# Performance work log

Hardware: AMD Instinct MI355X
Metric: run time of the kernel (lower is better)

## Reference

```python
import jax, jax.numpy as jnp
import numpy as np

DIM = 2048
N_HEADS = 16
HEAD_DIM = DIM // N_HEADS
MAX_SEQ_LEN = 2048
ROPE_THETA = 32.0
EPS = 1e-6


def _precompute_freqs_1d(dim, max_seq_len, theta):
    freqs = theta ** (-np.arange(0, dim, 2, dtype=np.float32) / dim)  # [dim/2]
    pos = np.arange(max_seq_len, dtype=np.float32)                    # [S]
    ang = pos[:, None] * freqs[None, :]                               # [S, dim/2]
    return jnp.asarray(np.cos(ang)), jnp.asarray(np.sin(ang))


def _rms_norm(x, w):
    # x: [..., d]
    inv = jax.lax.rsqrt(jnp.mean(x * x, axis=-1, keepdims=True) + EPS)
    return x * inv * w


def setup_inputs() -> dict:
    key = jax.random.key(0)
    k1, k2, k3 = jax.random.split(key, 3)
    bsz, seq_len = 4, 2048
    x = jax.random.normal(k1, (bsz, seq_len, DIM), dtype=jnp.float32)
    w_qkv = jax.random.normal(k2, (3 * DIM, DIM), dtype=jnp.float32) * (DIM ** -0.5)
    w_proj = jax.random.normal(k3, (DIM, DIM), dtype=jnp.float32) * (DIM ** -0.5)
    q_norm_w = jnp.ones((HEAD_DIM,), dtype=jnp.float32)
    k_norm_w = jnp.ones((HEAD_DIM,), dtype=jnp.float32)
    return {"x": x, "w_qkv": w_qkv, "w_proj": w_proj,
            "q_norm_w": q_norm_w, "k_norm_w": k_norm_w}


def reference(x, w_qkv, w_proj, q_norm_w, k_norm_w):
    bsz, seq_len, dim = x.shape
    scale = HEAD_DIM ** -0.5

    # QKV projection (torch Linear: x @ W^T)
    qkv = jnp.einsum('bsd,ed->bse', x, w_qkv)  # [b, s, 3*dim]
    qkv = qkv.reshape(bsz, seq_len, 3, N_HEADS, HEAD_DIM).transpose(2, 0, 3, 1, 4)
    q, k, v = qkv[0], qkv[1], qkv[2]           # each [b, h, s, d]

    # Per-head RMSNorm on q, k
    q = _rms_norm(q, q_norm_w)
    k = _rms_norm(k, k_norm_w)

    # RoPE (half-split convention)
    cos, sin = _precompute_freqs_1d(HEAD_DIM, MAX_SEQ_LEN, ROPE_THETA)
    cos = cos[:seq_len][None, None]  # [1,1,s,d/2]
    sin = sin[:seq_len][None, None]
    q1, q2 = jnp.split(q, 2, axis=-1)
    k1, k2 = jnp.split(k, 2, axis=-1)
    q = jnp.concatenate([q1 * cos - q2 * sin, q2 * cos + q1 * sin], axis=-1)
    k = jnp.concatenate([k1 * cos - k2 * sin, k2 * cos + k1 * sin], axis=-1)

    # Scaled dot-product attention (no mask, eval-mode: no dropout)
    scores = jnp.einsum('bhqd,bhkd->bhqk', q, k) * scale
    attn = jax.nn.softmax(scores, axis=-1)
    y = jnp.einsum('bhqk,bhkd->bhqd', attn, v)

    # Merge heads + output projection
    y = y.transpose(0, 2, 1, 3).reshape(bsz, seq_len, dim)
    return jnp.einsum('bsd,ed->bse', y, w_proj)
```

## Files before the change

kernel.cpp:

```cpp
#include <hip/hip_runtime.h>
#include <hip/hip_bf16.h>

#define BSZ 4
#define SEQ 2048
#define DIM 2048
#define NH 16
#define HD 128
#define QK_LD 4096
#define SCALE 0.08838834764831845f

typedef __attribute__((ext_vector_type(8))) short bf16x8;
typedef __attribute__((ext_vector_type(4))) float f32x4;

#define GLDS16(g, l)                                                           \
  __builtin_amdgcn_global_load_lds(                                           \
      (const __attribute__((address_space(1))) void*)(g),                     \
      (__attribute__((address_space(3))) void*)(l), 16, 0, 0)

__device__ inline short f2b(float f) {
  __hip_bfloat16 h = __float2bfloat16(f);
  short s;
  __builtin_memcpy(&s, &h, 2);
  return s;
}

__device__ inline void stage16(const float* gp, __hip_bfloat16* lp) {
  float4 q0 = ((const float4*)gp)[0], q1 = ((const float4*)gp)[1];
  float4 q2 = ((const float4*)gp)[2], q3 = ((const float4*)gp)[3];
  bf16x8 v0, v1;
  v0[0] = f2b(q0.x); v0[1] = f2b(q0.y); v0[2] = f2b(q0.z); v0[3] = f2b(q0.w);
  v0[4] = f2b(q1.x); v0[5] = f2b(q1.y); v0[6] = f2b(q1.z); v0[7] = f2b(q1.w);
  v1[0] = f2b(q2.x); v1[1] = f2b(q2.y); v1[2] = f2b(q2.z); v1[3] = f2b(q2.w);
  v1[4] = f2b(q3.x); v1[5] = f2b(q3.y); v1[6] = f2b(q3.z); v1[7] = f2b(q3.w);
  *(bf16x8*)lp = v0;
  *(bf16x8*)(lp + 8) = v1;
}

__device__ inline char* out_slice(void* outv, int b, int fl) {
  return (char*)outv + (size_t)b * (size_t)SEQ * DIM * (fl ? 2u : 4u);
}

__global__ __launch_bounds__(256)
void detect_canon(const unsigned int* __restrict__ wbits,
                  const void* __restrict__ qw, const void* __restrict__ kw,
                  __hip_bfloat16* __restrict__ qwb,
                  __hip_bfloat16* __restrict__ kwb, int* __restrict__ flag) {
  __shared__ int cnt;
  const int t = threadIdx.x;
  if (t == 0) cnt = 0;
  __syncthreads();
  int local = 0;
  for (int i = 0; i < 4; ++i) {
    unsigned int e = (wbits[t * 4 + i] >> 7) & 0xFF;
    if (e >= 96 && e < 160) local++;
  }
  atomicAdd(&cnt, local);
  __syncthreads();
  const int f = (cnt >= 768) ? 1 : 0;
  if (t == 0) *flag = f;
  if (t < 128)
    qwb[t] = f ? ((const __hip_bfloat16*)qw)[t]
               : __float2bfloat16(((const float*)qw)[t]);
  else
    kwb[t - 128] = f ? ((const __hip_bfloat16*)kw)[t - 128]
                     : __float2bfloat16(((const float*)kw)[t - 128]);
}

__global__ __launch_bounds__(256)
void convert_bf16(const void* __restrict__ in, __hip_bfloat16* __restrict__ out,
                  const int* __restrict__ flag) {
  const int fl = *flag;
  long i = ((long)blockIdx.x * 256 + threadIdx.x) * 8;
  if (fl) {
    *(float4*)(out + i) = *(const float4*)((const __hip_bfloat16*)in + i);
  } else {
    const float* p = (const float*)in + i;
    float4 a = ((const float4*)p)[0], b = ((const float4*)p)[1];
    bf16x8 o;
    o[0] = f2b(a.x); o[1] = f2b(a.y); o[2] = f2b(a.z); o[3] = f2b(a.w);
    o[4] = f2b(b.x); o[5] = f2b(b.y); o[6] = f2b(b.z); o[7] = f2b(b.w);
    *(bf16x8*)(out + i) = o;
  }
}


__global__ __launch_bounds__(256)
void gemm_qkv_full(const __hip_bfloat16* __restrict__ A,
                   const __hip_bfloat16* __restrict__ B,
                   __hip_bfloat16* __restrict__ qk, void* __restrict__ outv,
                   const int* __restrict__ flag) {
  __shared__ __hip_bfloat16 As[128 * 32];
  __shared__ __hip_bfloat16 Bs[128 * 32];
  const int t = threadIdx.x, wave = t >> 6, lane = t & 63;
  const int quad = lane >> 4, l16 = lane & 15;
  const int wm = (wave & 1) * 64, wn = (wave >> 1) * 64;
  const long bm = (long)blockIdx.x * 128, bn = (long)blockIdx.y * 128;
  const int fl = *flag;

  f32x4 acc[4][4] = {};
  for (int k0 = 0; k0 < DIM; k0 += 32) {
    __syncthreads();
    for (int i = 0; i < 2; ++i) {
      int c = wave * 64 + lane + i * 256;
      int row = c >> 2, kc = c & 3;
      GLDS16(A + (bm + row) * DIM + k0 + kc * 8, As + (wave * 64 + i * 256) * 8);
      GLDS16(B + (bn + row) * DIM + k0 + kc * 8, Bs + (wave * 64 + i * 256) * 8);
    }
    __syncthreads();
    bf16x8 aF[4], bF[4];
    for (int mt = 0; mt < 4; ++mt)
      aF[mt] = *(const bf16x8*)(As + (wm + mt * 16 + l16) * 32 + quad * 8);
    for (int nt = 0; nt < 4; ++nt)
      bF[nt] = *(const bf16x8*)(Bs + (wn + nt * 16 + l16) * 32 + quad * 8);
    for (int mt = 0; mt < 4; ++mt)
      for (int nt = 0; nt < 4; ++nt)
        acc[mt][nt] = __builtin_amdgcn_mfma_f32_16x16x32_bf16(
            aF[mt], bF[nt], acc[mt][nt], 0, 0, 0);
  }

  if (bn < 4096) {
    for (int mt = 0; mt < 4; ++mt) {
      long gr = bm + wm + mt * 16 + quad * 4;
      for (int nt = 0; nt < 4; ++nt) {
        long gc = bn + wn + nt * 16 + l16;
        for (int r = 0; r < 4; ++r)
          qk[(gr + r) * QK_LD + gc] = __float2bfloat16(acc[mt][nt][r]);
      }
    }
  } else {
    for (int mt = 0; mt < 4; ++mt) {
      long gr = bm + wm + mt * 16 + quad * 4;
      __hip_bfloat16* vtb = (__hip_bfloat16*)out_slice(outv, (int)(gr >> 11), fl);
      long s = gr & 2047;
      for (int nt = 0; nt < 4; ++nt) {
        long col = bn - 4096 + wn + nt * 16 + l16;
        for (int r = 0; r < 4; ++r)
          vtb[col * SEQ + s + r] = __float2bfloat16(acc[mt][nt][r]);
      }
    }
  }
}

__global__ __launch_bounds__(256)
void gemm_proj_full(const __hip_bfloat16* __restrict__ A,
                    const __hip_bfloat16* __restrict__ B,
                    void* __restrict__ outv, const int* __restrict__ flag) {
  __shared__ __hip_bfloat16 As[128 * 32];
  __shared__ __hip_bfloat16 Bs[128 * 32];
  const int t = threadIdx.x, wave = t >> 6, lane = t & 63;
  const int quad = lane >> 4, l16 = lane & 15;
  const int wm = (wave & 1) * 64, wn = (wave >> 1) * 64;
  const long bm = (long)blockIdx.x * 128, bn = (long)blockIdx.y * 128;
  const int fl = *flag;

  f32x4 acc[4][4] = {};
  for (int k0 = 0; k0 < DIM; k0 += 32) {
    __syncthreads();
    for (int i = 0; i < 2; ++i) {
      int c = wave * 64 + lane + i * 256;
      int row = c >> 2, kc = c & 3;
      GLDS16(A + (bm + row) * QK_LD + k0 + kc * 8, As + (wave * 64 + i * 256) * 8);
      GLDS16(B + (bn + row) * DIM + k0 + kc * 8, Bs + (wave * 64 + i * 256) * 8);
    }
    __syncthreads();
    bf16x8 aF[4], bF[4];
    for (int mt = 0; mt < 4; ++mt)
      aF[mt] = *(const bf16x8*)(As + (wm + mt * 16 + l16) * 32 + quad * 8);
    for (int nt = 0; nt < 4; ++nt)
      bF[nt] = *(const bf16x8*)(Bs + (wn + nt * 16 + l16) * 32 + quad * 8);
    for (int mt = 0; mt < 4; ++mt)
      for (int nt = 0; nt < 4; ++nt)
        acc[mt][nt] = __builtin_amdgcn_mfma_f32_16x16x32_bf16(
            aF[mt], bF[nt], acc[mt][nt], 0, 0, 0);
  }

  for (int mt = 0; mt < 4; ++mt) {
    long gr = bm + wm + mt * 16 + quad * 4;
    for (int nt = 0; nt < 4; ++nt) {
      long gc = bn + wn + nt * 16 + l16;
      for (int r = 0; r < 4; ++r) {
        long idx = (gr + r) * DIM + gc;
        if (fl) ((__hip_bfloat16*)outv)[idx] = __float2bfloat16(acc[mt][nt][r]);
        else    ((float*)outv)[idx] = acc[mt][nt][r];
      }
    }
  }
}


__global__ __launch_bounds__(256)
void gemm_qkv(const void* __restrict__ xin, const void* __restrict__ win,
              __hip_bfloat16* __restrict__ qk, void* __restrict__ outv,
              const int* __restrict__ flag, int b) {
  __shared__ __hip_bfloat16 As[128 * 32];
  __shared__ __hip_bfloat16 Bs[128 * 32];
  const int t = threadIdx.x, wave = t >> 6, lane = t & 63;
  const int quad = lane >> 4, l16 = lane & 15;
  const int wm = (wave & 1) * 64, wn = (wave >> 1) * 64;
  const long bm = (long)blockIdx.x * 128, bn = (long)blockIdx.y * 128;
  const int fl = *flag;
  const __hip_bfloat16* Ab = (const __hip_bfloat16*)xin + (long)b * SEQ * DIM;
  const __hip_bfloat16* Bb = (const __hip_bfloat16*)win;
  const float* Af = (const float*)xin + (long)b * SEQ * DIM;
  const float* Bf = (const float*)win;

  f32x4 acc[4][4] = {};
  for (int k0 = 0; k0 < DIM; k0 += 32) {
    __syncthreads();
    if (fl) {
      for (int i = 0; i < 2; ++i) {
        int c = wave * 64 + lane + i * 256;
        int row = c >> 2, kc = c & 3;
        GLDS16(Ab + (bm + row) * DIM + k0 + kc * 8, As + (wave * 64 + i * 256) * 8);
        GLDS16(Bb + (bn + row) * DIM + k0 + kc * 8, Bs + (wave * 64 + i * 256) * 8);
      }
    } else {
      int row = t >> 1, cb = k0 + (t & 1) * 16;
      stage16(Af + (bm + row) * DIM + cb, As + t * 16);
      stage16(Bf + (bn + row) * DIM + cb, Bs + t * 16);
    }
    __syncthreads();
    bf16x8 aF[4], bF[4];
    for (int mt = 0; mt < 4; ++mt)
      aF[mt] = *(const bf16x8*)(As + (wm + mt * 16 + l16) * 32 + quad * 8);
    for (int nt = 0; nt < 4; ++nt)
      bF[nt] = *(const bf16x8*)(Bs + (wn + nt * 16 + l16) * 32 + quad * 8);
    for (int mt = 0; mt < 4; ++mt)
      for (int nt = 0; nt < 4; ++nt)
        acc[mt][nt] = __builtin_amdgcn_mfma_f32_16x16x32_bf16(
            aF[mt], bF[nt], acc[mt][nt], 0, 0, 0);
  }

  if (bn < 4096) {
    for (int mt = 0; mt < 4; ++mt) {
      long gr = bm + wm + mt * 16 + quad * 4;
      for (int nt = 0; nt < 4; ++nt) {
        long gc = bn + wn + nt * 16 + l16;
        for (int r = 0; r < 4; ++r)
          qk[(gr + r) * QK_LD + gc] = __float2bfloat16(acc[mt][nt][r]);
      }
    }
  } else {
    __hip_bfloat16* vtb = (__hip_bfloat16*)out_slice(outv, b, fl);
    for (int mt = 0; mt < 4; ++mt) {
      long gr = bm + wm + mt * 16 + quad * 4;
      for (int nt = 0; nt < 4; ++nt) {
        long col = bn - 4096 + wn + nt * 16 + l16;
        for (int r = 0; r < 4; ++r)
          vtb[col * SEQ + gr + r] = __float2bfloat16(acc[mt][nt][r]);
      }
    }
  }
}

__global__ __launch_bounds__(256)
void gemm_proj(const __hip_bfloat16* __restrict__ A, const void* __restrict__ win,
               void* __restrict__ outv, const int* __restrict__ flag, int b) {
  __shared__ __hip_bfloat16 As[128 * 32];
  __shared__ __hip_bfloat16 Bs[128 * 32];
  const int t = threadIdx.x, wave = t >> 6, lane = t & 63;
  const int quad = lane >> 4, l16 = lane & 15;
  const int wm = (wave & 1) * 64, wn = (wave >> 1) * 64;
  const long bm = (long)blockIdx.x * 128, bn = (long)blockIdx.y * 128;
  const int fl = *flag;
  const __hip_bfloat16* Bb = (const __hip_bfloat16*)win;
  const float* Bf = (const float*)win;

  f32x4 acc[4][4] = {};
  for (int k0 = 0; k0 < DIM; k0 += 32) {
    __syncthreads();
    for (int i = 0; i < 2; ++i) {
      int c = wave * 64 + lane + i * 256;
      int row = c >> 2, kc = c & 3;
      GLDS16(A + (bm + row) * QK_LD + k0 + kc * 8, As + (wave * 64 + i * 256) * 8);
    }
    if (fl) {
      for (int i = 0; i < 2; ++i) {
        int c = wave * 64 + lane + i * 256;
        int row = c >> 2, kc = c & 3;
        GLDS16(Bb + (bn + row) * DIM + k0 + kc * 8, Bs + (wave * 64 + i * 256) * 8);
      }
    } else {
      int row = t >> 1, cb = k0 + (t & 1) * 16;
      stage16(Bf + (bn + row) * DIM + cb, Bs + t * 16);
    }
    __syncthreads();
    bf16x8 aF[4], bF[4];
    for (int mt = 0; mt < 4; ++mt)
      aF[mt] = *(const bf16x8*)(As + (wm + mt * 16 + l16) * 32 + quad * 8);
    for (int nt = 0; nt < 4; ++nt)
      bF[nt] = *(const bf16x8*)(Bs + (wn + nt * 16 + l16) * 32 + quad * 8);
    for (int mt = 0; mt < 4; ++mt)
      for (int nt = 0; nt < 4; ++nt)
        acc[mt][nt] = __builtin_amdgcn_mfma_f32_16x16x32_bf16(
            aF[mt], bF[nt], acc[mt][nt], 0, 0, 0);
  }

  char* Cb = out_slice(outv, b, fl);
  for (int mt = 0; mt < 4; ++mt) {
    long gr = bm + wm + mt * 16 + quad * 4;
    for (int nt = 0; nt < 4; ++nt) {
      long gc = bn + wn + nt * 16 + l16;
      for (int r = 0; r < 4; ++r) {
        long idx = (gr + r) * DIM + gc;
        if (fl) ((__hip_bfloat16*)Cb)[idx] = __float2bfloat16(acc[mt][nt][r]);
        else    ((float*)Cb)[idx] = acc[mt][nt][r];
      }
    }
  }
}


__global__ __launch_bounds__(256)
void norm_rope(__hip_bfloat16* __restrict__ qk,
               const __hip_bfloat16* __restrict__ qwb,
               const __hip_bfloat16* __restrict__ kwb) {
  const int wave = threadIdx.x >> 6, lane = threadIdx.x & 63;
  const int gid = blockIdx.x * 4 + wave;
  const int h = gid & 15, tt = (gid >> 4) & 1, row = gid >> 5;
  const int s = row & 2047;

  __hip_bfloat16* p = qk + (long)row * QK_LD + tt * DIM + h * HD;
  float v1 = __bfloat162float(p[lane]);
  float v2 = __bfloat162float(p[lane + 64]);

  float ss = v1 * v1 + v2 * v2;
  for (int off = 1; off < 64; off <<= 1) ss += __shfl_xor(ss, off);
  float inv = rsqrtf(ss * (1.0f / 128.0f) + 1e-6f);

  const __hip_bfloat16* w = tt ? kwb : qwb;
  float n1 = v1 * inv * __bfloat162float(w[lane]);
  float n2 = v2 * inv * __bfloat162float(w[lane + 64]);

  float freq = exp2f(-5.0f * (float)lane * (1.0f / 64.0f));
  float ang = (float)s * freq;
  float c = cosf(ang), sn = sinf(ang);

  p[lane]      = __float2bfloat16(n1 * c - n2 * sn);
  p[lane + 64] = __float2bfloat16(n2 * c + n1 * sn);
}

__global__ __launch_bounds__(256)
void flash_attn(__hip_bfloat16* __restrict__ qk, void* __restrict__ outv,
                const int* __restrict__ flag, int b) {
  __shared__ __hip_bfloat16 Qs[4 * 64 * 32];
  __shared__ __hip_bfloat16 Ks[4 * 64 * 32];
  __shared__ __hip_bfloat16 Vs[2 * 128 * 32];
  __shared__ __hip_bfloat16 Ps[4][2 * 16 * 32];

  const int t = threadIdx.x, wave = t >> 6, lane = t & 63;
  const int quad = lane >> 4, l16 = lane & 15;
  const int q0 = blockIdx.x * 64, h = blockIdx.y;
  const int fl = *flag;
  __hip_bfloat16* Qg = qk + h * HD;
  const __hip_bfloat16* Kg = Qg + DIM;
  const __hip_bfloat16* Vt =
      (const __hip_bfloat16*)out_slice(outv, b, fl) + (long)h * HD * SEQ;

  for (int i = 0; i < 4; ++i) {
    int f = wave * 64 + lane + i * 256;
    int kk = f & 3, row = (f >> 2) & 63, ks = f >> 8;
    GLDS16(Qg + (long)(q0 + row) * QK_LD + ks * 32 + kk * 8,
           Qs + (wave * 64 + i * 256) * 8);
  }

  f32x4 oacc[8] = {};
  float m_run[4], l_run[4];
  for (int r = 0; r < 4; ++r) { m_run[r] = -1e30f; l_run[r] = 0.0f; }

  for (int j0 = 0; j0 < SEQ; j0 += 64) {
    __syncthreads();
    for (int i = 0; i < 4; ++i) {
      int f = wave * 64 + lane + i * 256;
      int kk = f & 3, row = (f >> 2) & 63, ks = f >> 8;
      GLDS16(Kg + (long)(j0 + row) * QK_LD + ks * 32 + kk * 8,
             Ks + (wave * 64 + i * 256) * 8);
    }
    for (int i = 0; i < 4; ++i) {
      int f = wave * 64 + lane + i * 256;
      int kk = f & 3, dimr = (f >> 2) & 127, ks2 = f >> 9;
      GLDS16(Vt + (long)dimr * SEQ + j0 + ks2 * 32 + kk * 8,
             Vs + (wave * 64 + i * 256) * 8);
    }
    __syncthreads();

    f32x4 sacc[4] = {};
    for (int ks = 0; ks < 4; ++ks) {
      bf16x8 aQ = *(const bf16x8*)(Qs + (ks * 64 + wave * 16 + l16) * 32 + quad * 8);
      for (int nt = 0; nt < 4; ++nt) {
        bf16x8 bK = *(const bf16x8*)(Ks + (ks * 64 + nt * 16 + l16) * 32 + quad * 8);
        sacc[nt] = __builtin_amdgcn_mfma_f32_16x16x32_bf16(aQ, bK, sacc[nt], 0, 0, 0);
      }
    }

    float p[4][4];
    for (int r = 0; r < 4; ++r) {
      float mx = -1e30f;
      for (int nt = 0; nt < 4; ++nt) {
        float sv = sacc[nt][r] * SCALE;
        p[nt][r] = sv;
        mx = fmaxf(mx, sv);
      }
      for (int off = 1; off < 16; off <<= 1) mx = fmaxf(mx, __shfl_xor(mx, off));
      float mnew = fmaxf(m_run[r], mx);
      float sum = 0.0f;
      for (int nt = 0; nt < 4; ++nt) {
        float e = __expf(p[nt][r] - mnew);
        p[nt][r] = e;
        sum += e;
      }
      for (int off = 1; off < 16; off <<= 1) sum += __shfl_xor(sum, off);
      float alpha = __expf(m_run[r] - mnew);
      l_run[r] = l_run[r] * alpha + sum;
      m_run[r] = mnew;
      for (int n = 0; n < 8; ++n) oacc[n][r] = oacc[n][r] * alpha;
    }

    __hip_bfloat16* pw = &Ps[wave][0];
    for (int r = 0; r < 4; ++r)
      for (int nt = 0; nt < 4; ++nt)
        pw[((nt >> 1) * 16 + quad * 4 + r) * 32 + (nt & 1) * 16 + l16] =
            __float2bfloat16(p[nt][r]);
    __syncthreads();

    for (int ks2 = 0; ks2 < 2; ++ks2) {
      bf16x8 aP = *(const bf16x8*)(pw + (ks2 * 16 + l16) * 32 + quad * 8);
      for (int n = 0; n < 8; ++n) {
        bf16x8 bV = *(const bf16x8*)(Vs + (ks2 * 128 + n * 16 + l16) * 32 + quad * 8);
        oacc[n] = __builtin_amdgcn_mfma_f32_16x16x32_bf16(aP, bV, oacc[n], 0, 0, 0);
      }
    }
  }

  for (int r = 0; r < 4; ++r) {
    float rl = 1.0f / l_run[r];
    long s = q0 + wave * 16 + quad * 4 + r;
    for (int n = 0; n < 8; ++n)
      qk[s * QK_LD + h * HD + n * 16 + l16] = __float2bfloat16(oacc[n][r] * rl);
  }
}

extern "C" void kernel_launch(void* const* d_in, const int* in_sizes, int n_in,
                              void* d_out, int out_size, void* d_ws, size_t ws_size,
                              hipStream_t stream) {
  int* flag = (int*)d_ws;
  __hip_bfloat16* qwb = (__hip_bfloat16*)((char*)d_ws + 64);
  __hip_bfloat16* kwb = qwb + 128;
  char* base = (char*)d_ws + 1024;

  detect_canon<<<1, 256, 0, stream>>>((const unsigned int*)d_in[1], d_in[3],
                                      d_in[4], qwb, kwb, flag);

  const size_t MB = 1024ull * 1024ull;
  const size_t NEED_A = 1024 + 128 * MB;

  if (ws_size >= NEED_A) {
    __hip_bfloat16* xb     = (__hip_bfloat16*)base;
    __hip_bfloat16* wqkvb  = (__hip_bfloat16*)(base + 32 * MB);
    __hip_bfloat16* wprojb = (__hip_bfloat16*)(base + 56 * MB);
    __hip_bfloat16* qk     = (__hip_bfloat16*)(base + 64 * MB);

    convert_bf16<<<(BSZ * SEQ * DIM) / 2048, 256, 0, stream>>>(d_in[0], xb, flag);
    convert_bf16<<<(3 * DIM * DIM) / 2048, 256, 0, stream>>>(d_in[1], wqkvb, flag);
    convert_bf16<<<(DIM * DIM) / 2048, 256, 0, stream>>>(d_in[2], wprojb, flag);

    gemm_qkv_full<<<dim3((BSZ * SEQ) / 128, (3 * DIM) / 128), 256, 0, stream>>>(
        xb, wqkvb, qk, d_out, flag);
    norm_rope<<<(BSZ * SEQ * 2 * NH) / 4, 256, 0, stream>>>(qk, qwb, kwb);
    for (int b = 0; b < BSZ; ++b)
      flash_attn<<<dim3(SEQ / 64, NH), 256, 0, stream>>>(
          qk + (long)b * SEQ * QK_LD, d_out, flag, b);
    gemm_proj_full<<<dim3((BSZ * SEQ) / 128, DIM / 128), 256, 0, stream>>>(
        qk, wprojb, d_out, flag);
  } else {
    __hip_bfloat16* qk = (__hip_bfloat16*)base;
    for (int b = 0; b < BSZ; ++b) {
      gemm_qkv<<<dim3(SEQ / 128, (3 * DIM) / 128), 256, 0, stream>>>(
          d_in[0], d_in[1], qk, d_out, flag, b);
      norm_rope<<<(SEQ * 2 * NH) / 4, 256, 0, stream>>>(qk, qwb, kwb);
      flash_attn<<<dim3(SEQ / 64, NH), 256, 0, stream>>>(qk, d_out, flag, b);
      gemm_proj<<<dim3(SEQ / 128, DIM / 128), 256, 0, stream>>>(
          qk, d_in[2], d_out, flag, b);
    }
  }
}
```

Measured before the change: 916.9 us.

## Enlarge flash-attention query tile, keep Q in registers, batch launches, vectorize norm_rope

Flash attention now processes 128 query rows per block (32 per wave as two 16-row MFMA tiles), so each K/V tile loaded into LDS is reused across twice as many queries. Q fragments are read straight from global into registers instead of staged in LDS. The per-batch launch loop becomes a single 3D grid launch. norm_rope switches to 32-bit loads and stores, using lane shuffles to de-interleave and re-interleave the bf16 pairs. Together these raise register pressure and halve the number of blocks per batch, which can reduce occupancy.

```diff
diff --git a/kernel.cpp b/kernel.cpp
--- a/kernel.cpp
+++ b/kernel.cpp
@@ -321,8 +321,12 @@
   const int s = row & 2047;
 
   __hip_bfloat16* p = qk + (long)row * QK_LD + tt * DIM + h * HD;
-  float v1 = __bfloat162float(p[lane]);
-  float v2 = __bfloat162float(p[lane + 64]);
+  unsigned int u = ((const unsigned int*)p)[lane];
+
+  unsigned int x = (unsigned int)__shfl((int)u, lane >> 1);
+  unsigned int y = (unsigned int)__shfl((int)u, 32 + (lane >> 1));
+  float v1 = __uint_as_float((lane & 1) ? (x & 0xFFFF0000u) : (x << 16));
+  float v2 = __uint_as_float((lane & 1) ? (y & 0xFFFF0000u) : (y << 16));
 
   float ss = v1 * v1 + v2 * v2;
   for (int off = 1; off < 64; off <<= 1) ss += __shfl_xor(ss, off);
@@ -335,38 +339,49 @@
   float freq = exp2f(-5.0f * (float)lane * (1.0f / 64.0f));
   float ang = (float)s * freq;
   float c = cosf(ang), sn = sinf(ang);
-
-  p[lane]      = __float2bfloat16(n1 * c - n2 * sn);
-  p[lane + 64] = __float2bfloat16(n2 * c + n1 * sn);
-}
-
-__global__ __launch_bounds__(256)
-void flash_attn(__hip_bfloat16* __restrict__ qk, void* __restrict__ outv,
-                const int* __restrict__ flag, int b) {
-  __shared__ __hip_bfloat16 Qs[4 * 64 * 32];
+  float r1 = n1 * c - n2 * sn;
+  float r2 = n2 * c + n1 * sn;
+
+  float z1lo = __shfl(r1, (2 * lane) & 63), z2lo = __shfl(r2, (2 * lane) & 63);
+  float z1hi = __shfl(r1, (2 * lane + 1) & 63), z2hi = __shfl(r2, (2 * lane + 1) & 63);
+  float lo = (lane < 32) ? z1lo : z2lo;
+  float hi = (lane < 32) ? z1hi : z2hi;
+  unsigned int ou = (unsigned int)(unsigned short)f2b(lo) |
+                    ((unsigned int)(unsigned short)f2b(hi) << 16);
+  ((unsigned int*)p)[lane] = ou;
+}
+
+__global__ __launch_bounds__(256)
+void flash_attn(__hip_bfloat16* __restrict__ qkbase, void* __restrict__ outv,
+                const int* __restrict__ flag, int b0) {
   __shared__ __hip_bfloat16 Ks[4 * 64 * 32];
   __shared__ __hip_bfloat16 Vs[2 * 128 * 32];
-  __shared__ __hip_bfloat16 Ps[4][2 * 16 * 32];
+  __shared__ __hip_bfloat16 Ps[4][2 * 32 * 32];
 
   const int t = threadIdx.x, wave = t >> 6, lane = t & 63;
   const int quad = lane >> 4, l16 = lane & 15;
-  const int q0 = blockIdx.x * 64, h = blockIdx.y;
+  const int q0 = blockIdx.x * 128, h = blockIdx.y;
+  const int b = b0 + blockIdx.z;
   const int fl = *flag;
+  __hip_bfloat16* qk = qkbase + (long)blockIdx.z * SEQ * QK_LD;
   __hip_bfloat16* Qg = qk + h * HD;
   const __hip_bfloat16* Kg = Qg + DIM;
   const __hip_bfloat16* Vt =
       (const __hip_bfloat16*)out_slice(outv, b, fl) + (long)h * HD * SEQ;
 
-  for (int i = 0; i < 4; ++i) {
-    int f = wave * 64 + lane + i * 256;
-    int kk = f & 3, row = (f >> 2) & 63, ks = f >> 8;
-    GLDS16(Qg + (long)(q0 + row) * QK_LD + ks * 32 + kk * 8,
-           Qs + (wave * 64 + i * 256) * 8);
-  }
-
-  f32x4 oacc[8] = {};
-  float m_run[4], l_run[4];
-  for (int r = 0; r < 4; ++r) { m_run[r] = -1e30f; l_run[r] = 0.0f; }
+  bf16x8 aQ[2][4];
+#pragma unroll
+  for (int mt = 0; mt < 2; ++mt)
+#pragma unroll
+    for (int ks = 0; ks < 4; ++ks)
+      aQ[mt][ks] = *(const bf16x8*)(Qg +
+          (long)(q0 + wave * 32 + mt * 16 + l16) * QK_LD + ks * 32 + quad * 8);
+
+  f32x4 oacc[2][8] = {};
+  float m_run[2][4], l_run[2][4];
+#pragma unroll
+  for (int mt = 0; mt < 2; ++mt)
+    for (int r = 0; r < 4; ++r) { m_run[mt][r] = -1e30f; l_run[mt][r] = 0.0f; }
 
   for (int j0 = 0; j0 < SEQ; j0 += 64) {
     __syncthreads();
@@ -384,60 +399,75 @@
     }
     __syncthreads();
 
-    f32x4 sacc[4] = {};
-    for (int ks = 0; ks < 4; ++ks) {
-      bf16x8 aQ = *(const bf16x8*)(Qs + (ks * 64 + wave * 16 + l16) * 32 + quad * 8);
+    f32x4 sacc[2][4] = {};
+#pragma unroll
+    for (int ks = 0; ks < 4; ++ks)
+#pragma unroll
       for (int nt = 0; nt < 4; ++nt) {
         bf16x8 bK = *(const bf16x8*)(Ks + (ks * 64 + nt * 16 + l16) * 32 + quad * 8);
-        sacc[nt] = __builtin_amdgcn_mfma_f32_16x16x32_bf16(aQ, bK, sacc[nt], 0, 0, 0);
-      }
-    }
-
-    float p[4][4];
-    for (int r = 0; r < 4; ++r) {
-      float mx = -1e30f;
-      for (int nt = 0; nt < 4; ++nt) {
-        float sv = sacc[nt][r] * SCALE;
-        p[nt][r] = sv;
-        mx = fmaxf(mx, sv);
-      }
-      for (int off = 1; off < 16; off <<= 1) mx = fmaxf(mx, __shfl_xor(mx, off));
-      float mnew = fmaxf(m_run[r], mx);
-      float sum = 0.0f;
-      for (int nt = 0; nt < 4; ++nt) {
-        float e = __expf(p[nt][r] - mnew);
-        p[nt][r] = e;
-        sum += e;
-      }
-      for (int off = 1; off < 16; off <<= 1) sum += __shfl_xor(sum, off);
-      float alpha = __expf(m_run[r] - mnew);
-      l_run[r] = l_run[r] * alpha + sum;
-      m_run[r] = mnew;
-      for (int n = 0; n < 8; ++n) oacc[n][r] = oacc[n][r] * alpha;
-    }
+#pragma unroll
+        for (int mt = 0; mt < 2; ++mt)
+          sacc[mt][nt] = __builtin_amdgcn_mfma_f32_16x16x32_bf16(
+              aQ[mt][ks], bK, sacc[mt][nt], 0, 0, 0);
+      }
 
     __hip_bfloat16* pw = &Ps[wave][0];
-    for (int r = 0; r < 4; ++r)
-      for (int nt = 0; nt < 4; ++nt)
-        pw[((nt >> 1) * 16 + quad * 4 + r) * 32 + (nt & 1) * 16 + l16] =
-            __float2bfloat16(p[nt][r]);
-    __syncthreads();
-
+#pragma unroll
+    for (int mt = 0; mt < 2; ++mt) {
+      float p[4][4];
+      for (int r = 0; r < 4; ++r) {
+        float mx = -1e30f;
+        for (int nt = 0; nt < 4; ++nt) {
+          float sv = sacc[mt][nt][r] * SCALE;
+          p[nt][r] = sv;
+          mx = fmaxf(mx, sv);
+        }
+        for (int off = 1; off < 16; off <<= 1) mx = fmaxf(mx, __shfl_xor(mx, off));
+        float mnew = fmaxf(m_run[mt][r], mx);
+        float sum = 0.0f;
+        for (int nt = 0; nt < 4; ++nt) {
+          float e = __expf(p[nt][r] - mnew);
+          p[nt][r] = e;
+          sum += e;
+        }
+        for (int off = 1; off < 16; off <<= 1) sum += __shfl_xor(sum, off);
+        float alpha = __expf(m_run[mt][r] - mnew);
+        l_run[mt][r] = l_run[mt][r] * alpha + sum;
+        m_run[mt][r] = mnew;
+        for (int n = 0; n < 8; ++n) oacc[mt][n][r] = oacc[mt][n][r] * alpha;
+      }
+      for (int r = 0; r < 4; ++r)
+        for (int nt = 0; nt < 4; ++nt)
+          pw[((nt >> 1) * 32 + mt * 16 + quad * 4 + r) * 32 + (nt & 1) * 16 + l16] =
+              __float2bfloat16(p[nt][r]);
+    }
+
+#pragma unroll
     for (int ks2 = 0; ks2 < 2; ++ks2) {
-      bf16x8 aP = *(const bf16x8*)(pw + (ks2 * 16 + l16) * 32 + quad * 8);
+      bf16x8 aP[2];
+#pragma unroll
+      for (int mt = 0; mt < 2; ++mt)
+        aP[mt] = *(const bf16x8*)(pw + (ks2 * 32 + mt * 16 + l16) * 32 + quad * 8);
+#pragma unroll
       for (int n = 0; n < 8; ++n) {
         bf16x8 bV = *(const bf16x8*)(Vs + (ks2 * 128 + n * 16 + l16) * 32 + quad * 8);
-        oacc[n] = __builtin_amdgcn_mfma_f32_16x16x32_bf16(aP, bV, oacc[n], 0, 0, 0);
-      }
-    }
-  }
-
-  for (int r = 0; r < 4; ++r) {
-    float rl = 1.0f / l_run[r];
-    long s = q0 + wave * 16 + quad * 4 + r;
-    for (int n = 0; n < 8; ++n)
-      qk[s * QK_LD + h * HD + n * 16 + l16] = __float2bfloat16(oacc[n][r] * rl);
-  }
+#pragma unroll
+        for (int mt = 0; mt < 2; ++mt)
+          oacc[mt][n] = __builtin_amdgcn_mfma_f32_16x16x32_bf16(
+              aP[mt], bV, oacc[mt][n], 0, 0, 0);
+      }
+    }
+  }
+
+#pragma unroll
+  for (int mt = 0; mt < 2; ++mt)
+    for (int r = 0; r < 4; ++r) {
+      float rl = 1.0f / l_run[mt][r];
+      long s = q0 + wave * 32 + mt * 16 + quad * 4 + r;
+      for (int n = 0; n < 8; ++n)
+        qk[s * QK_LD + h * HD + n * 16 + l16] =
+            __float2bfloat16(oacc[mt][n][r] * rl);
+    }
 }
 
 extern "C" void kernel_launch(void* const* d_in, const int* in_sizes, int n_in,
@@ -467,9 +497,7 @@
     gemm_qkv_full<<<dim3((BSZ * SEQ) / 128, (3 * DIM) / 128), 256, 0, stream>>>(
         xb, wqkvb, qk, d_out, flag);
     norm_rope<<<(BSZ * SEQ * 2 * NH) / 4, 256, 0, stream>>>(qk, qwb, kwb);
-    for (int b = 0; b < BSZ; ++b)
-      flash_attn<<<dim3(SEQ / 64, NH), 256, 0, stream>>>(
-          qk + (long)b * SEQ * QK_LD, d_out, flag, b);
+    flash_attn<<<dim3(SEQ / 128, NH, BSZ), 256, 0, stream>>>(qk, d_out, flag, 0);
     gemm_proj_full<<<dim3((BSZ * SEQ) / 128, DIM / 128), 256, 0, stream>>>(
         qk, wprojb, d_out, flag);
   } else {
@@ -478,7 +506,7 @@
       gemm_qkv<<<dim3(SEQ / 128, (3 * DIM) / 128), 256, 0, stream>>>(
           d_in[0], d_in[1], qk, d_out, flag, b);
       norm_rope<<<(SEQ * 2 * NH) / 4, 256, 0, stream>>>(qk, qwb, kwb);
-      flash_attn<<<dim3(SEQ / 64, NH), 256, 0, stream>>>(qk, d_out, flag, b);
+      flash_attn<<<dim3(SEQ / 128, NH, 1), 256, 0, stream>>>(qk, d_out, flag, b);
       gemm_proj<<<dim3(SEQ / 128, DIM / 128), 256, 0, stream>>>(
           qk, d_in[2], d_out, flag, b);
     }
```

New measurement: 863.5 us. 5.8% less time.
